# Performance work log

Hardware: AMD Instinct MI355X
Metric: run time of the kernel (lower is better)

The kernel has to match this reference:

```python
import jax, jax.numpy as jnp
import numpy as np

BATCH = 2
L = 2048
D_MODEL = 1024
D_STATE = 16
D_CONV = 4
EXPAND = 2
D_INNER = EXPAND * D_MODEL  # 2048
DT_RANK = (D_MODEL + 15) // 16  # 64


def setup_inputs() -> dict:
    key = jax.random.key(0)
    ks = jax.random.split(key, 12)
    f = jnp.float32
    hidden_states = jax.random.normal(ks[0], (BATCH, L, D_MODEL), f)
    input2 = jax.random.normal(ks[1], (BATCH, L, D_MODEL), f)
    in_proj1_w = jax.random.normal(ks[2], (D_INNER, D_MODEL), f) * (D_MODEL ** -0.5)
    in_proj2_w = jax.random.normal(ks[3], (D_INNER, D_MODEL), f) * (D_MODEL ** -0.5)
    conv_w = jax.random.normal(ks[4], (D_INNER, 1, D_CONV), f) * (D_CONV ** -0.5)
    conv_b = jax.random.normal(ks[5], (D_INNER,), f) * 0.02
    x_proj_w = jax.random.normal(ks[6], (DT_RANK + 2 * D_STATE, D_INNER), f) * (D_INNER ** -0.5)
    dt_std = DT_RANK ** -0.5
    dt_proj_w = jax.random.uniform(ks[7], (D_INNER, DT_RANK), f, -dt_std, dt_std)
    # dt bias init: inverse softplus of log-uniform dt in [1e-3, 1e-1]
    dt = jnp.exp(jax.random.uniform(ks[8], (D_INNER,), f) * (np.log(0.1) - np.log(0.001)) + np.log(0.001))
    dt = jnp.clip(dt, 1e-4, None)
    dt_proj_b = dt + jnp.log(-jnp.expm1(-dt))
    # A_log init: log(1..d_state) broadcast over channels
    A_log = jnp.log(jnp.broadcast_to(jnp.arange(1, D_STATE + 1, dtype=f), (D_INNER, D_STATE)))
    D = jnp.ones((D_INNER,), f)
    out_proj_w = jax.random.normal(ks[9], (D_MODEL, D_INNER), f) * (D_INNER ** -0.5)
    return dict(hidden_states=hidden_states, input2=input2, in_proj1_w=in_proj1_w,
                in_proj2_w=in_proj2_w, conv_w=conv_w, conv_b=conv_b, x_proj_w=x_proj_w,
                dt_proj_w=dt_proj_w, dt_proj_b=dt_proj_b, A_log=A_log, D=D,
                out_proj_w=out_proj_w)


def _forward(hidden_states, input2, in_proj1_w, in_proj2_w, conv_w, conv_b,
             x_proj_w, dt_proj_w, dt_proj_b, A_log, D, out_proj_w):
    # in_proj: (B,L,Dm) -> (B,d_inner,L)
    x = jnp.einsum('bld,ed->bel', hidden_states, in_proj1_w)
    z = jnp.einsum('bld,ed->bel', input2, in_proj2_w)
    # causal depthwise conv1d (left pad d_conv-1, equiv to torch pad+truncate) + SiLU
    xc = jax.lax.conv_general_dilated(x, conv_w, (1,), [(D_CONV - 1, 0)],
                                      dimension_numbers=('NCH', 'OIH', 'NCH'),
                                      feature_group_count=D_INNER)
    x = jax.nn.silu(xc + conv_b[None, :, None])
    # x_proj -> dt, B, C
    x_dbl = jnp.einsum('bel,re->brl', x, x_proj_w)  # (B, dt_rank+2n, L)
    dt = x_dbl[:, :DT_RANK]
    Bm = x_dbl[:, DT_RANK:DT_RANK + D_STATE]       # (B, n, L)
    Cm = x_dbl[:, DT_RANK + D_STATE:]               # (B, n, L)
    delta = jnp.einsum('brl,er->bel', dt, dt_proj_w)
    delta = jax.nn.softplus(delta + dt_proj_b[None, :, None])  # (B, d_inner, L)
    A = -jnp.exp(A_log)  # (d_inner, n)
    # selective scan over time (time-major for lax.scan)
    dlt = jnp.transpose(delta, (2, 0, 1))  # (L, B, d)
    u = jnp.transpose(x, (2, 0, 1))        # (L, B, d)
    Bt = jnp.transpose(Bm, (2, 0, 1))      # (L, B, n)
    Ct = jnp.transpose(Cm, (2, 0, 1))      # (L, B, n)

    def step(state, inp):
        d_t, u_t, B_t, C_t = inp
        dA = jnp.exp(d_t[..., None] * A)                        # (B, d, n)
        state = state * dA + (d_t * u_t)[..., None] * B_t[:, None, :]
        y_t = jnp.einsum('bdn,bn->bd', state, C_t)
        return state, y_t

    init = jnp.zeros((hidden_states.shape[0], D_INNER, D_STATE), x.dtype)
    _, ys = jax.lax.scan(step, init, (dlt, u, Bt, Ct))
    y = jnp.transpose(ys, (1, 2, 0)) + D[None, :, None] * x  # (B, d, L)
    y = y * jax.nn.silu(z)
    out = jnp.einsum('bel,de->bld', y, out_proj_w)  # out_proj, no bias
    return out


def reference(hidden_states, input2, in_proj1_w, in_proj2_w, conv_w, conv_b,
              x_proj_w, dt_proj_w, dt_proj_b, A_log, D, out_proj_w):
    return _forward(hidden_states, input2, in_proj1_w, in_proj2_w, conv_w, conv_b,
                    x_proj_w, dt_proj_w, dt_proj_b, A_log, D, out_proj_w)
```

## Files before the change

kernel.cpp:

```cpp
#include <hip/hip_runtime.h>
#include <cstddef>
#include <cmath>

#define BATCH 2
#define LSEQ 2048
#define DM 1024
#define DSTATE 16
#define DI 2048
#define DTR 64
#define XDR 96
#define NC 64
#define TC 32
#define PN (4096 * 96)

using f32x4 = __attribute__((ext_vector_type(4))) float;
using bf16x8 = __attribute__((ext_vector_type(8))) short;

__device__ __forceinline__ unsigned short f2bf(float f) {
  union { float f; unsigned int u; } c; c.f = f;
  unsigned int u = c.u;
  return (unsigned short)((u + 0x7FFFu + ((u >> 16) & 1u)) >> 16);
}
__device__ __forceinline__ float bf2f(unsigned short h) {
  union { unsigned int u; float f; } c; c.u = ((unsigned int)h) << 16;
  return c.f;
}
__device__ __forceinline__ unsigned int pack2(float a, float b) {
  return (unsigned int)f2bf(a) | ((unsigned int)f2bf(b) << 16);
}

__device__ __forceinline__ void gl_lds16(const void* g, void* l) {
  __builtin_amdgcn_global_load_lds(
      (const __attribute__((address_space(1))) void*)g,
      (__attribute__((address_space(3))) void*)l, 16, 0, 0);
}

__device__ __forceinline__ float softplus_fast(float x) {
  float ex = __expf(x);
  return (x > 20.f) ? x : __logf(1.f + ex);
}

__device__ __forceinline__ void pow_tree(float q1, float* dA) {
  float q2 = q1 * q1;
  float q3 = q2 * q1;
  float q4 = q2 * q2;
  float q8 = q4 * q4;
  float q5 = q4 * q1, q6 = q4 * q2, q7 = q4 * q3;
  dA[0] = q1;  dA[1] = q2;  dA[2] = q3;  dA[3] = q4;
  dA[4] = q5;  dA[5] = q6;  dA[6] = q7;  dA[7] = q8;
  dA[8] = q8 * q1;  dA[9] = q8 * q2;  dA[10] = q8 * q3;  dA[11] = q8 * q4;
  dA[12] = q8 * q5; dA[13] = q8 * q6; dA[14] = q8 * q7;  dA[15] = q8 * q8;
}

#define G_HS   524288
#define G_IN2  (G_HS + 524288)
#define G_W1   (G_IN2 + 262144)
#define G_W2   (G_W1 + 262144)
#define G_XPW  (G_W2 + 24576)
#define G_DTW  (G_XPW + 16384)
#define G_OW   (G_DTW + 262144)

__global__ __launch_bounds__(256) void cvt_all_kernel(
    const float* __restrict__ hs, const float* __restrict__ in2,
    const float* __restrict__ w1, const float* __restrict__ w2,
    const float* __restrict__ xpw, const float* __restrict__ dtw,
    const float* __restrict__ ow, unsigned short* __restrict__ hsb,
    unsigned short* __restrict__ in2b, unsigned short* __restrict__ wb1,
    unsigned short* __restrict__ wb2, unsigned short* __restrict__ xpwB,
    unsigned short* __restrict__ dtwB, unsigned short* __restrict__ owb) {
  int i = blockIdx.x * 256 + threadIdx.x;
  const float* s;
  unsigned short* d;
  int k;
  if (i < G_HS)       { s = hs;  d = hsb;  k = i; }
  else if (i < G_IN2) { s = in2; d = in2b; k = i - G_HS; }
  else if (i < G_W1)  { s = w1;  d = wb1;  k = i - G_IN2; }
  else if (i < G_W2)  { s = w2;  d = wb2;  k = i - G_W1; }
  else if (i < G_XPW) { s = xpw; d = xpwB; k = i - G_W2; }
  else if (i < G_DTW) { s = dtw; d = dtwB; k = i - G_XPW; }
  else                { s = ow;  d = owb;  k = i - G_DTW; }
  const float4* sp = reinterpret_cast<const float4*>(s) + (size_t)k * 2;
  float4 a = sp[0], b = sp[1];
  uint4 v = make_uint4(pack2(a.x, a.y), pack2(a.z, a.w), pack2(b.x, b.y),
                       pack2(b.z, b.w));
  *(reinterpret_cast<uint4*>(d) + k) = v;
}

__global__ __launch_bounds__(512) void gemm_in12(
    const unsigned short* __restrict__ A0, const unsigned short* __restrict__ B0,
    unsigned short* __restrict__ C0, const unsigned short* __restrict__ A1,
    const unsigned short* __restrict__ B1, unsigned short* __restrict__ C1) {
  __shared__ __align__(16) unsigned short Asm[2][256][64];
  __shared__ __align__(16) unsigned short Bsm[2][256][64];

  const unsigned short* A = blockIdx.z ? A1 : A0;
  const unsigned short* B = blockIdx.z ? B1 : B0;
  unsigned short* C = blockIdx.z ? C1 : C0;
  const int lda = DM, ldc = DI;

  const int tid = threadIdx.x;
  const int lane = tid & 63;
  const int w = tid >> 6;
  const int wr = w >> 2;
  const int wn = w & 3;

  const int gx = gridDim.x;
  const int nwg = gx * gridDim.y;
  const int id = blockIdx.y * gx + blockIdx.x;
  const int cpx = nwg >> 3;
  const int lt = (id & 7) * cpx + (id >> 3);
  const size_t m0 = (size_t)(lt / gx) * 256;
  const size_t n0 = (size_t)(lt % gx) * 256;

  const int rsub = lane >> 3;
  const int sslot = (lane & 7) ^ rsub;
  const unsigned short* Ab = A + (m0 + (size_t)rsub) * lda + sslot * 8;
  const unsigned short* Bb = B + (n0 + (size_t)rsub) * lda + sslot * 8;

  const int fr = lane & 15;
  const int q = lane >> 4;
  const int f7 = fr & 7;

  f32x4 acc[8][4] = {};
  bf16x8 bfr[4][2];

#define STA(BUF, T)                                                         \
  {                                                                         \
    const int r0_ = w * 32;                                                 \
    const unsigned short* s_ = Ab + (size_t)r0_ * lda + (T) * 64;           \
    gl_lds16(s_, &Asm[BUF][r0_][0]);                                        \
    gl_lds16(s_ + (size_t)8 * lda, &Asm[BUF][r0_ + 8][0]);                  \
    gl_lds16(s_ + (size_t)16 * lda, &Asm[BUF][r0_ + 16][0]);                \
    gl_lds16(s_ + (size_t)24 * lda, &Asm[BUF][r0_ + 24][0]);                \
  }
#define STB(BUF, T)                                                         \
  {                                                                         \
    const int r0_ = w * 32;                                                 \
    const unsigned short* s_ = Bb + (size_t)r0_ * lda + (T) * 64;           \
    gl_lds16(s_, &Bsm[BUF][r0_][0]);                                        \
    gl_lds16(s_ + (size_t)8 * lda, &Bsm[BUF][r0_ + 8][0]);                  \
    gl_lds16(s_ + (size_t)16 * lda, &Bsm[BUF][r0_ + 16][0]);                \
    gl_lds16(s_ + (size_t)24 * lda, &Bsm[BUF][r0_ + 24][0]);                \
  }

#define PH4(BUFI, HALF, LOADB, STG, VM)                                     \
  {                                                                         \
    if (LOADB) {                                                            \
      _Pragma("unroll") for (int j = 0; j < 4; ++j)                         \
          _Pragma("unroll") for (int kk = 0; kk < 2; ++kk)                  \
              bfr[j][kk] = *reinterpret_cast<const bf16x8*>(                \
                  &Bsm[BUFI][wn * 64 + j * 16 + fr]                         \
                      [((kk * 4 + q) ^ f7) << 3]);                          \
    }                                                                       \
    bf16x8 af_[4][2];                                                       \
    _Pragma("unroll") for (int mi = 0; mi < 4; ++mi)                        \
        _Pragma("unroll") for (int kk = 0; kk < 2; ++kk)                    \
            af_[mi][kk] = *reinterpret_cast<const bf16x8*>(                 \
                &Asm[BUFI][wr * 128 + ((HALF)*4 + mi) * 16 + fr]            \
                    [((kk * 4 + q) ^ f7) << 3]);                            \
    STG;                                                                    \
    VM;                                                                     \
    __builtin_amdgcn_s_barrier();                                           \
    asm volatile("s_waitcnt lgkmcnt(0)" ::: "memory");                      \
    __builtin_amdgcn_sched_barrier(0);                                      \
    __builtin_amdgcn_s_setprio(1);                                          \
    _Pragma("unroll") for (int kk = 0; kk < 2; ++kk)                        \
        _Pragma("unroll") for (int mi = 0; mi < 4; ++mi)                    \
            _Pragma("unroll") for (int j = 0; j < 4; ++j)                   \
                acc[(HALF)*4 + mi][j] =                                     \
                    __builtin_amdgcn_mfma_f32_16x16x32_bf16(                \
                        af_[mi][kk], bfr[j][kk], acc[(HALF)*4 + mi][j],     \
                        0, 0, 0);                                           \
    __builtin_amdgcn_s_setprio(0);                                          \
    __builtin_amdgcn_s_barrier();                                           \
  }

#define VMC4_ asm volatile("s_waitcnt vmcnt(4)" ::: "memory")
#define VMC0_ asm volatile("s_waitcnt vmcnt(0)" ::: "memory")
#define NOPS_ ((void)0)

  STB(0, 0)
  STA(0, 0)
  STB(1, 1)
  VMC4_;
  __builtin_amdgcn_s_barrier();

#pragma unroll 1
  for (int it = 0; it < 7; ++it) {
    const int t0 = 2 * it, t1 = 2 * it + 1;
    PH4(0, 0, true,  STA(1, t1),     NOPS_)
    PH4(0, 1, false, STB(0, t0 + 2), VMC4_)
    PH4(1, 0, true,  STA(0, t0 + 2), NOPS_)
    PH4(1, 1, false, STB(1, t1 + 2), VMC4_)
  }
  PH4(0, 0, true,  STA(1, 15), NOPS_)
  PH4(0, 1, false, NOPS_,      VMC0_)
  PH4(1, 0, true,  NOPS_, NOPS_)
  PH4(1, 1, false, NOPS_, NOPS_)

#undef STA
#undef STB
#undef PH4

  const int crb = q * 4;
#pragma unroll
  for (int mf = 0; mf < 8; ++mf) {
    size_t row = m0 + wr * 128 + mf * 16 + crb;
#pragma unroll
    for (int j = 0; j < 4; ++j) {
      size_t col = n0 + wn * 64 + j * 16 + fr;
#pragma unroll
      for (int r = 0; r < 4; ++r)
        C[(row + r) * ldc + col] = f2bf(acc[mf][j][r]);
    }
  }
}

__global__ __launch_bounds__(256) void gemm_out(
    const unsigned short* __restrict__ A, const unsigned short* __restrict__ B,
    float* __restrict__ C) {
  __shared__ __align__(16) unsigned short As[128][64];
  __shared__ __align__(16) unsigned short Bs[64][64];

  const int K = DI, lda = DI, ldb = DI, ldc = DM;

  const int tid = threadIdx.x;
  const int lane = tid & 63;
  const int w = tid >> 6;

  const int gx = gridDim.x;
  const int nwg = gx * gridDim.y;
  const int id = blockIdx.y * gx + blockIdx.x;
  const int cpx = nwg >> 3;
  const int lt = (id & 7) * cpx + (id >> 3);
  const size_t m0 = (size_t)(lt / gx) * 128;
  const size_t n0 = (size_t)(lt % gx) * 64;

  const int rsub = lane >> 3;
  const int sslot = (lane & 7) ^ rsub;
  const unsigned short* Ab = A + m0 * lda + (size_t)rsub * lda + sslot * 8;
  const unsigned short* Bb = B + n0 * ldb + (size_t)rsub * ldb + sslot * 8;

  f32x4 acc[4][2] = {};

  const int fr = lane & 15;
  const int q = lane >> 4;
  const int f7 = fr & 7;

  for (int k0 = 0; k0 < K; k0 += 64) {
#pragma unroll
    for (int i = 0; i < 4; ++i) {
      const int r0 = w * 32 + i * 8;
      gl_lds16(Ab + (size_t)r0 * lda + k0, &As[r0][0]);
    }
#pragma unroll
    for (int i = 0; i < 2; ++i) {
      const int r0 = w * 16 + i * 8;
      gl_lds16(Bb + (size_t)r0 * ldb + k0, &Bs[r0][0]);
    }
    __syncthreads();

    bf16x8 af[4][2], bf_[2][2];
#pragma unroll
    for (int kk = 0; kk < 2; ++kk) {
      const int sA = (((kk * 4 + q) ^ f7) << 3);
#pragma unroll
      for (int i = 0; i < 4; ++i)
        af[i][kk] = *reinterpret_cast<const bf16x8*>(
            &As[(w >> 1) * 64 + i * 16 + fr][sA]);
#pragma unroll
      for (int j = 0; j < 2; ++j)
        bf_[j][kk] = *reinterpret_cast<const bf16x8*>(
            &Bs[(w & 1) * 32 + j * 16 + fr][sA]);
    }
#pragma unroll
    for (int kk = 0; kk < 2; ++kk)
#pragma unroll
      for (int i = 0; i < 4; ++i)
#pragma unroll
        for (int j = 0; j < 2; ++j)
          acc[i][j] = __builtin_amdgcn_mfma_f32_16x16x32_bf16(
              af[i][kk], bf_[j][kk], acc[i][j], 0, 0, 0);
    __syncthreads();
  }

  const int crb = q * 4;
#pragma unroll
  for (int i = 0; i < 4; ++i) {
    size_t row = m0 + (w >> 1) * 64 + i * 16 + crb;
#pragma unroll
    for (int j = 0; j < 2; ++j) {
      size_t col = n0 + (w & 1) * 32 + j * 16 + fr;
#pragma unroll
      for (int r = 0; r < 4; ++r)
        C[(row + r) * ldc + col] = acc[i][j][r];
    }
  }
}

__global__ __launch_bounds__(256) void gemm_delta(
    const unsigned short* __restrict__ A, const unsigned short* __restrict__ B,
    const float* __restrict__ bias, unsigned short* __restrict__ C, int K,
    int lda, int ldb, int ldc) {
  __shared__ __align__(16) unsigned short As[128][64];
  __shared__ __align__(16) unsigned short Bs[128][64];

  const int tid = threadIdx.x;
  const int lane = tid & 63;
  const int w = tid >> 6;

  const int gx = gridDim.x;
  const int nwg = gx * gridDim.y;
  const int id = blockIdx.y * gx + blockIdx.x;
  const int cpx = nwg >> 3;
  const int lt = (id & 7) * cpx + (id >> 3);
  const size_t m0 = (size_t)(lt / gx) * 128;
  const size_t n0 = (size_t)(lt % gx) * 128;

  const int rsub = lane >> 3;
  const int sslot = (lane & 7) ^ rsub;
  const unsigned short* Ab = A + m0 * lda + (size_t)rsub * lda + sslot * 8;
  const unsigned short* Bb = B + n0 * ldb + (size_t)rsub * ldb + sslot * 8;

  f32x4 acc[4][4] = {};

  const int fr = lane & 15;
  const int q = lane >> 4;
  const int f7 = fr & 7;

  for (int k0 = 0; k0 < K; k0 += 64) {
#pragma unroll
    for (int i = 0; i < 4; ++i) {
      const int r0 = w * 32 + i * 8;
      gl_lds16(Ab + (size_t)r0 * lda + k0, &As[r0][0]);
      gl_lds16(Bb + (size_t)r0 * ldb + k0, &Bs[r0][0]);
    }
    __syncthreads();

    bf16x8 af[4][2], bf_[4][2];
#pragma unroll
    for (int i = 0; i < 4; ++i) {
#pragma unroll
      for (int kk = 0; kk < 2; ++kk) {
        const int sA = (((kk * 4 + q) ^ f7) << 3);
        af[i][kk] = *reinterpret_cast<const bf16x8*>(
            &As[(w >> 1) * 64 + i * 16 + fr][sA]);
        bf_[i][kk] = *reinterpret_cast<const bf16x8*>(
            &Bs[(w & 1) * 64 + i * 16 + fr][sA]);
      }
    }
#pragma unroll
    for (int kk = 0; kk < 2; ++kk)
#pragma unroll
      for (int i = 0; i < 4; ++i)
#pragma unroll
        for (int j = 0; j < 4; ++j)
          acc[i][j] = __builtin_amdgcn_mfma_f32_16x16x32_bf16(
              af[i][kk], bf_[j][kk], acc[i][j], 0, 0, 0);
    __syncthreads();
  }

  const int crb = q * 4;
#pragma unroll
  for (int i = 0; i < 4; ++i) {
    size_t row = m0 + (w >> 1) * 64 + i * 16 + crb;
#pragma unroll
    for (int j = 0; j < 4; ++j) {
      size_t col = n0 + (w & 1) * 64 + j * 16 + fr;
      float bv = bias[col];
#pragma unroll
      for (int r = 0; r < 4; ++r)
        C[(row + r) * ldc + col] = f2bf(softplus_fast(acc[i][j][r] + bv));
    }
  }
}

__global__ __launch_bounds__(256) void gemm_xdbl(
    const unsigned short* __restrict__ A,
    const unsigned short* __restrict__ B,
    float* __restrict__ P) {
  __shared__ __align__(16) unsigned short As[128][64];
  __shared__ __align__(16) unsigned short Bs[96][64];

  const int tid = threadIdx.x;
  const int lane = tid & 63;
  const int w = tid >> 6;
  const size_t m0 = (size_t)blockIdx.x * 128;
  const int k0base = blockIdx.y * 256;

  const int rsub = lane >> 3;
  const int sslot = (lane & 7) ^ rsub;
  const unsigned short* Ab = A + m0 * DI + (size_t)rsub * DI + sslot * 8;
  const unsigned short* Bb = B + (size_t)rsub * DI + sslot * 8;

  f32x4 acc[4][3] = {};

  const int fr = lane & 15;
  const int q = lane >> 4;
  const int f7 = fr & 7;

  for (int ks = 0; ks < 4; ++ks) {
    const int k0 = k0base + ks * 64;
#pragma unroll
    for (int i = 0; i < 4; ++i) {
      const int r0 = w * 32 + i * 8;
      gl_lds16(Ab + (size_t)r0 * DI + k0, &As[r0][0]);
    }
#pragma unroll
    for (int i = 0; i < 3; ++i) {
      const int r0 = w * 24 + i * 8;
      gl_lds16(Bb + (size_t)r0 * DI + k0, &Bs[r0][0]);
    }
    __syncthreads();

    bf16x8 af[4][2], bf_[3][2];
#pragma unroll
    for (int kk = 0; kk < 2; ++kk) {
      const int sA = (((kk * 4 + q) ^ f7) << 3);
#pragma unroll
      for (int i = 0; i < 4; ++i)
        af[i][kk] = *reinterpret_cast<const bf16x8*>(
            &As[(w >> 1) * 64 + i * 16 + fr][sA]);
#pragma unroll
      for (int j = 0; j < 3; ++j)
        bf_[j][kk] = *reinterpret_cast<const bf16x8*>(
            &Bs[(w & 1) * 48 + j * 16 + fr][sA]);
    }
#pragma unroll
    for (int kk = 0; kk < 2; ++kk)
#pragma unroll
      for (int i = 0; i < 4; ++i)
#pragma unroll
        for (int j = 0; j < 3; ++j)
          acc[i][j] = __builtin_amdgcn_mfma_f32_16x16x32_bf16(
              af[i][kk], bf_[j][kk], acc[i][j], 0, 0, 0);
    __syncthreads();
  }

  float* Pz = P + (size_t)blockIdx.y * PN;
  const int crb = q * 4;
#pragma unroll
  for (int i = 0; i < 4; ++i) {
    size_t row = m0 + (w >> 1) * 64 + i * 16 + crb;
#pragma unroll
    for (int j = 0; j < 3; ++j) {
      int col = (w & 1) * 48 + j * 16 + fr;
#pragma unroll
      for (int r = 0; r < 4; ++r) Pz[(row + r) * XDR + col] = acc[i][j][r];
    }
  }
}

__global__ __launch_bounds__(256) void reduce8x_kernel(
    const float* __restrict__ P, unsigned short* __restrict__ dtB,
    float* __restrict__ BC) {
  int i = blockIdx.x * 256 + threadIdx.x;
  int row = i / XDR, col = i - row * XDR;
  float s01 = P[i] + P[PN + i];
  float s23 = P[2 * PN + i] + P[3 * PN + i];
  float s45 = P[4 * PN + i] + P[5 * PN + i];
  float s67 = P[6 * PN + i] + P[7 * PN + i];
  float s = (s01 + s23) + (s45 + s67);
  if (col < 64)
    dtB[row * 64 + col] = f2bf(s);
  else
    BC[row * 32 + (col - 64)] = s;
}

__global__ __launch_bounds__(256) void conv_silu_kernel(
    const unsigned short* __restrict__ x, const float* __restrict__ w,
    const float* __restrict__ cb, unsigned short* __restrict__ out) {
  int idx = blockIdx.x * 256 + threadIdx.x;
  int e4 = idx % (DI / 4);
  int bl = idx / (DI / 4);
  int l = bl % LSEQ;
  int e = e4 * 4;

  const float4* cw = reinterpret_cast<const float4*>(w);
  float4 w0 = cw[e], w1 = cw[e + 1], w2 = cw[e + 2], w3 = cw[e + 3];
  float4 acc = *reinterpret_cast<const float4*>(&cb[e]);

#define TAPK(K, COMP)                                                       \
  {                                                                         \
    int ls = l - 3 + (K);                                                   \
    if (ls >= 0) {                                                          \
      uint2 xv = *reinterpret_cast<const uint2*>(                           \
          &x[((size_t)(bl) - 3 + (K)) * DI + e]);                           \
      acc.x = fmaf(bf2f((unsigned short)(xv.x & 0xffff)), w0.COMP, acc.x);  \
      acc.y = fmaf(bf2f((unsigned short)(xv.x >> 16)), w1.COMP, acc.y);     \
      acc.z = fmaf(bf2f((unsigned short)(xv.y & 0xffff)), w2.COMP, acc.z);  \
      acc.w = fmaf(bf2f((unsigned short)(xv.y >> 16)), w3.COMP, acc.w);     \
    }                                                                       \
  }
  TAPK(0, x)
  TAPK(1, y)
  TAPK(2, z)
  TAPK(3, w)
#undef TAPK

  acc.x = acc.x / (1.f + __expf(-acc.x));
  acc.y = acc.y / (1.f + __expf(-acc.y));
  acc.z = acc.z / (1.f + __expf(-acc.z));
  acc.w = acc.w / (1.f + __expf(-acc.w));
  *reinterpret_cast<uint2*>(&out[(size_t)bl * DI + e]) =
      make_uint2(pack2(acc.x, acc.y), pack2(acc.z, acc.w));
}

__global__ __launch_bounds__(256) void scan_passA(
    const unsigned short* __restrict__ dB, const unsigned short* __restrict__ u,
    const float* __restrict__ bc, const float* __restrict__ A_log,
    float* __restrict__ sEnd, float* __restrict__ sProd) {
  int g = blockIdx.x * 256 + threadIdx.x;
  int e = g & (DI - 1);
  int c = (g >> 11) & (NC - 1);
  int b = g >> 17;

  const float nA0 = -__expf(A_log[e * DSTATE]);
  bool aok = true;
#pragma unroll
  for (int n = 1; n < DSTATE; ++n) {
    float nAn = -__expf(A_log[e * DSTATE + n]);
    aok = aok && (fabsf(nAn - (float)(n + 1) * nA0) <= 1e-4f * fabsf(nAn));
  }

  size_t off = ((size_t)b * LSEQ + c * TC) * DI + e;
  size_t boff = ((size_t)b * LSEQ + c * TC) * 32;

  float s[DSTATE], P[DSTATE];
#pragma unroll
  for (int n = 0; n < DSTATE; ++n) { s[n] = 0.f; P[n] = 1.f; }
  float sumd = 0.f;

  float d = bf2f(dB[off]);
  float ut = bf2f(u[off]);

  for (int t = 0; t < TC; ++t) {
    float d_n = 0.f, ut_n = 0.f;
    if (t + 1 < TC) {
      d_n = bf2f(dB[off + DI]);
      ut_n = bf2f(u[off + DI]);
    }

    float db = d * ut;
    float dA[DSTATE];
    if (aok) {
      pow_tree(__expf(d * nA0), dA);
      sumd += d;
    } else {
#pragma unroll
      for (int n = 0; n < DSTATE; ++n) {
        dA[n] = __expf(-d * __expf(A_log[e * DSTATE + n]));
        P[n] *= dA[n];
      }
    }
    const float4* bcp = reinterpret_cast<const float4*>(&bc[boff]);
    float4 B0 = bcp[0], B1 = bcp[1], B2 = bcp[2], B3 = bcp[3];
    float Bv[DSTATE] = {B0.x, B0.y, B0.z, B0.w, B1.x, B1.y, B1.z, B1.w,
                        B2.x, B2.y, B2.z, B2.w, B3.x, B3.y, B3.z, B3.w};
#pragma unroll
    for (int n = 0; n < DSTATE; ++n)
      s[n] = fmaf(s[n], dA[n], db * Bv[n]);
    off += DI;
    boff += 32;
    d = d_n; ut = ut_n;
  }

  if (aok) pow_tree(__expf(sumd * nA0), P);

  size_t o = (((size_t)b * NC + c) * DI + e) * DSTATE;
  float4* se = reinterpret_cast<float4*>(&sEnd[o]);
  float4* sp = reinterpret_cast<float4*>(&sProd[o]);
  se[0] = make_float4(s[0], s[1], s[2], s[3]);
  se[1] = make_float4(s[4], s[5], s[6], s[7]);
  se[2] = make_float4(s[8], s[9], s[10], s[11]);
  se[3] = make_float4(s[12], s[13], s[14], s[15]);
  sp[0] = make_float4(P[0], P[1], P[2], P[3]);
  sp[1] = make_float4(P[4], P[5], P[6], P[7]);
  sp[2] = make_float4(P[8], P[9], P[10], P[11]);
  sp[3] = make_float4(P[12], P[13], P[14], P[15]);
}

__global__ __launch_bounds__(256) void scan_passB(
    float* __restrict__ sEnd, const float* __restrict__ sProd) {
  int g = blockIdx.x * 256 + threadIdx.x;
  int n = g & 15;
  int e = (g >> 4) & (DI - 1);
  int b = g >> 15;
  float s = 0.f;
  for (int c = 0; c < NC; ++c) {
    size_t o = (((size_t)b * NC + c) * DI + e) * DSTATE + n;
    float se = sEnd[o];
    float sp = sProd[o];
    sEnd[o] = s;
    s = fmaf(s, sp, se);
  }
}

__global__ __launch_bounds__(256) void scan_passC(
    const unsigned short* __restrict__ dB, const unsigned short* __restrict__ u,
    const unsigned short* __restrict__ z, const float* __restrict__ bc,
    const float* __restrict__ A_log, const float* __restrict__ Dv,
    const float* __restrict__ sInit, unsigned short* __restrict__ gOut) {
  int g = blockIdx.x * 256 + threadIdx.x;
  int e = g & (DI - 1);
  int c = (g >> 11) & (NC - 1);
  int b = g >> 17;

  const float nA0 = -__expf(A_log[e * DSTATE]);
  bool aok = true;
#pragma unroll
  for (int n = 1; n < DSTATE; ++n) {
    float nAn = -__expf(A_log[e * DSTATE + n]);
    aok = aok && (fabsf(nAn - (float)(n + 1) * nA0) <= 1e-4f * fabsf(nAn));
  }
  const float Dval = Dv[e];

  size_t off = ((size_t)b * LSEQ + c * TC) * DI + e;
  size_t boff = ((size_t)b * LSEQ + c * TC) * 32;

  float s[DSTATE];
  {
    size_t o = (((size_t)b * NC + c) * DI + e) * DSTATE;
    const float4* si = reinterpret_cast<const float4*>(&sInit[o]);
    float4 s0 = si[0], s1 = si[1], s2 = si[2], s3 = si[3];
    s[0] = s0.x; s[1] = s0.y; s[2] = s0.z; s[3] = s0.w;
    s[4] = s1.x; s[5] = s1.y; s[6] = s1.z; s[7] = s1.w;
    s[8] = s2.x; s[9] = s2.y; s[10] = s2.z; s[11] = s2.w;
    s[12] = s3.x; s[13] = s3.y; s[14] = s3.z; s[15] = s3.w;
  }

  float d = bf2f(dB[off]);
  float ut = bf2f(u[off]);
  float zt = bf2f(z[off]);

  for (int t = 0; t < TC; ++t) {
    float d_n = 0.f, ut_n = 0.f, zt_n = 0.f;
    if (t + 1 < TC) {
      d_n = bf2f(dB[off + DI]);
      ut_n = bf2f(u[off + DI]);
      zt_n = bf2f(z[off + DI]);
    }

    float db = d * ut;
    float dA[DSTATE];
    if (aok) {
      pow_tree(__expf(d * nA0), dA);
    } else {
#pragma unroll
      for (int n = 0; n < DSTATE; ++n)
        dA[n] = __expf(-d * __expf(A_log[e * DSTATE + n]));
    }
    const float4* bcp = reinterpret_cast<const float4*>(&bc[boff]);
    float4 B0 = bcp[0], B1 = bcp[1], B2 = bcp[2], B3 = bcp[3];
    float4 C0 = bcp[4], C1 = bcp[5], C2 = bcp[6], C3 = bcp[7];
    float Bv[DSTATE] = {B0.x, B0.y, B0.z, B0.w, B1.x, B1.y, B1.z, B1.w,
                        B2.x, B2.y, B2.z, B2.w, B3.x, B3.y, B3.z, B3.w};
    float Cv[DSTATE] = {C0.x, C0.y, C0.z, C0.w, C1.x, C1.y, C1.z, C1.w,
                        C2.x, C2.y, C2.z, C2.w, C3.x, C3.y, C3.z, C3.w};
    float y0 = 0.f, y1 = 0.f, y2 = 0.f, y3 = 0.f;
#pragma unroll
    for (int n = 0; n < 4; ++n) {
      s[n] = fmaf(s[n], dA[n], db * Bv[n]);
      y0 = fmaf(s[n], Cv[n], y0);
      s[n + 4] = fmaf(s[n + 4], dA[n + 4], db * Bv[n + 4]);
      y1 = fmaf(s[n + 4], Cv[n + 4], y1);
      s[n + 8] = fmaf(s[n + 8], dA[n + 8], db * Bv[n + 8]);
      y2 = fmaf(s[n + 8], Cv[n + 8], y2);
      s[n + 12] = fmaf(s[n + 12], dA[n + 12], db * Bv[n + 12]);
      y3 = fmaf(s[n + 12], Cv[n + 12], y3);
    }
    float y = (y0 + y1) + (y2 + y3);
    float gate = zt / (1.f + __expf(-zt));
    gOut[off] = f2bf((y + Dval * ut) * gate);

    off += DI;
    boff += 32;
    d = d_n; ut = ut_n; zt = zt_n;
  }
}

extern "C" void kernel_launch(void* const* d_in, const int* in_sizes, int n_in,
                              void* d_out, int out_size, void* d_ws,
                              size_t ws_size, hipStream_t stream) {
  const float* hs = (const float*)d_in[0];
  const float* in2 = (const float*)d_in[1];
  const float* w1 = (const float*)d_in[2];
  const float* w2 = (const float*)d_in[3];
  const float* cw = (const float*)d_in[4];
  const float* cb = (const float*)d_in[5];
  const float* xpw = (const float*)d_in[6];
  const float* dtw = (const float*)d_in[7];
  const float* dtb = (const float*)d_in[8];
  const float* alog = (const float*)d_in[9];
  const float* Dv = (const float*)d_in[10];
  const float* ow = (const float*)d_in[11];
  float* out = (float*)d_out;

  const size_t BLE = (size_t)BATCH * LSEQ * DI;
  const size_t WN = (size_t)DI * DM;
  const size_t SC = (size_t)BATCH * NC * DI * DSTATE;

  float* W = (float*)d_ws;
  float* bufX = W;
  float* M2 = W + BLE;
  float* M3 = M2 + BLE / 2;
  float* M4 = M3 + BLE / 2;
  float* sEnd = M4 + BLE / 2;
  float* sProd = sEnd + SC;
  float* BC = sProd + SC;
  float* DED = BC + 131072;

  unsigned short* xpreB = (unsigned short*)bufX;
  unsigned short* dB = (unsigned short*)bufX;
  unsigned short* hsb = (unsigned short*)M2;
  unsigned short* zb = (unsigned short*)M2;
  unsigned short* in2b = (unsigned short*)M3;
  unsigned short* ub = (unsigned short*)M3;
  unsigned short* wb1 = (unsigned short*)M4;
  unsigned short* wb2 = wb1 + WN;
  float* xdblP = M4;
  unsigned short* dtB = (unsigned short*)(M4 + 8 * PN);
  unsigned short* bufG = (unsigned short*)M4;
  unsigned short* owb = (unsigned short*)DED;
  unsigned short* xpwB = owb + WN;
  unsigned short* dtwB = xpwB + XDR * DI;

  const int M = BATCH * LSEQ;
  dim3 blk(256);

  cvt_all_kernel<<<G_OW / 256, blk, 0, stream>>>(hs, in2, w1, w2, xpw, dtw, ow,
                                                 hsb, in2b, wb1, wb2, xpwB,
                                                 dtwB, owb);
  gemm_in12<<<dim3(DI / 256, M / 256, 2), dim3(512), 0, stream>>>(
      hsb, wb1, xpreB, in2b, wb2, zb);
  conv_silu_kernel<<<(M * (DI / 4)) / 256, blk, 0, stream>>>(xpreB, cw, cb,
                                                             ub);
  gemm_xdbl<<<dim3(M / 128, 8), blk, 0, stream>>>(ub, xpwB, xdblP);
  reduce8x_kernel<<<(M * XDR) / 256, blk, 0, stream>>>(xdblP, dtB, BC);
  gemm_delta<<<dim3(DI / 128, M / 128), blk, 0, stream>>>(
      dtB, dtwB, dtb, dB, DTR, DTR, DTR, DI);
  scan_passA<<<(BATCH * DI * NC) / 256, blk, 0, stream>>>(dB, ub, BC, alog,
                                                          sEnd, sProd);
  scan_passB<<<(BATCH * DI * DSTATE) / 256, blk, 0, stream>>>(sEnd, sProd);
  scan_passC<<<(BATCH * DI * NC) / 256, blk, 0, stream>>>(
      dB, ub, zb, BC, alog, Dv, sEnd, bufG);
  gemm_out<<<dim3(DM / 64, M / 128), blk, 0, stream>>>(bufG, owb, out);
}
```

Before: 214.9 us.

## Double-buffer out-projection GEMM with 512-thread 256x64 tiles and prefetch pipeline

Rewrites gemm_out to use 512 threads on a 256x64 output tile with two LDS buffers, prefetching the next K-tiles while MFMAs run on the current one. Explicit waitcnt, barriers and setprio schedule the loads against the compute. The intent is to hide global load latency and halve the number of workgroups. The grid falls to 256 blocks, which may underfill the GPU, and the hand-tuned vmcnt values are fragile.

```diff
diff --git a/kernel.cpp b/kernel.cpp
--- a/kernel.cpp
+++ b/kernel.cpp
@@ -216,84 +216,114 @@
   }
 }
 
-__global__ __launch_bounds__(256) void gemm_out(
+__global__ __launch_bounds__(512) void gemm_out(
     const unsigned short* __restrict__ A, const unsigned short* __restrict__ B,
     float* __restrict__ C) {
-  __shared__ __align__(16) unsigned short As[128][64];
-  __shared__ __align__(16) unsigned short Bs[64][64];
-
-  const int K = DI, lda = DI, ldb = DI, ldc = DM;
+  __shared__ __align__(16) unsigned short Asm[2][256][64];
+  __shared__ __align__(16) unsigned short Bsm[2][64][64];
+
+  const int lda = DI, ldc = DM;
 
   const int tid = threadIdx.x;
   const int lane = tid & 63;
   const int w = tid >> 6;
+  const int wm = w >> 1;
+  const int wn = w & 1;
 
   const int gx = gridDim.x;
   const int nwg = gx * gridDim.y;
   const int id = blockIdx.y * gx + blockIdx.x;
   const int cpx = nwg >> 3;
   const int lt = (id & 7) * cpx + (id >> 3);
-  const size_t m0 = (size_t)(lt / gx) * 128;
+  const size_t m0 = (size_t)(lt / gx) * 256;
   const size_t n0 = (size_t)(lt % gx) * 64;
 
   const int rsub = lane >> 3;
   const int sslot = (lane & 7) ^ rsub;
-  const unsigned short* Ab = A + m0 * lda + (size_t)rsub * lda + sslot * 8;
-  const unsigned short* Bb = B + n0 * ldb + (size_t)rsub * ldb + sslot * 8;
-
-  f32x4 acc[4][2] = {};
+  const unsigned short* Ab = A + (m0 + (size_t)rsub) * lda + sslot * 8;
+  const unsigned short* Bb = B + (n0 + (size_t)rsub) * lda + sslot * 8;
 
   const int fr = lane & 15;
   const int q = lane >> 4;
   const int f7 = fr & 7;
 
-  for (int k0 = 0; k0 < K; k0 += 64) {
-#pragma unroll
-    for (int i = 0; i < 4; ++i) {
-      const int r0 = w * 32 + i * 8;
-      gl_lds16(Ab + (size_t)r0 * lda + k0, &As[r0][0]);
-    }
-#pragma unroll
-    for (int i = 0; i < 2; ++i) {
-      const int r0 = w * 16 + i * 8;
-      gl_lds16(Bb + (size_t)r0 * ldb + k0, &Bs[r0][0]);
-    }
-    __syncthreads();
-
-    bf16x8 af[4][2], bf_[2][2];
-#pragma unroll
-    for (int kk = 0; kk < 2; ++kk) {
-      const int sA = (((kk * 4 + q) ^ f7) << 3);
-#pragma unroll
-      for (int i = 0; i < 4; ++i)
-        af[i][kk] = *reinterpret_cast<const bf16x8*>(
-            &As[(w >> 1) * 64 + i * 16 + fr][sA]);
-#pragma unroll
-      for (int j = 0; j < 2; ++j)
-        bf_[j][kk] = *reinterpret_cast<const bf16x8*>(
-            &Bs[(w & 1) * 32 + j * 16 + fr][sA]);
-    }
-#pragma unroll
-    for (int kk = 0; kk < 2; ++kk)
-#pragma unroll
-      for (int i = 0; i < 4; ++i)
-#pragma unroll
-        for (int j = 0; j < 2; ++j)
-          acc[i][j] = __builtin_amdgcn_mfma_f32_16x16x32_bf16(
-              af[i][kk], bf_[j][kk], acc[i][j], 0, 0, 0);
-    __syncthreads();
-  }
+  f32x4 acc[4][2] = {};
+
+#define OSTA(BUF, T)                                                        \
+  {                                                                         \
+    const int r0_ = w * 32;                                                 \
+    const unsigned short* s_ = Ab + (size_t)r0_ * lda + (T) * 64;           \
+    gl_lds16(s_, &Asm[BUF][r0_][0]);                                        \
+    gl_lds16(s_ + (size_t)8 * lda, &Asm[BUF][r0_ + 8][0]);                  \
+    gl_lds16(s_ + (size_t)16 * lda, &Asm[BUF][r0_ + 16][0]);                \
+    gl_lds16(s_ + (size_t)24 * lda, &Asm[BUF][r0_ + 24][0]);                \
+  }
+#define OSTB(BUF, T)                                                        \
+  {                                                                         \
+    const int r0_ = w * 8;                                                  \
+    gl_lds16(Bb + (size_t)r0_ * lda + (T) * 64, &Bsm[BUF][r0_][0]);         \
+  }
+
+#define OPH(BUFI, STG, VM)                                                  \
+  {                                                                         \
+    bf16x8 af_[4][2], bf_[2][2];                                            \
+    _Pragma("unroll") for (int j = 0; j < 2; ++j)                           \
+        _Pragma("unroll") for (int kk = 0; kk < 2; ++kk)                    \
+            bf_[j][kk] = *reinterpret_cast<const bf16x8*>(                  \
+                &Bsm[BUFI][wn * 32 + j * 16 + fr]                           \
+                    [((kk * 4 + q) ^ f7) << 3]);                            \
+    _Pragma("unroll") for (int mi = 0; mi < 4; ++mi)                        \
+        _Pragma("unroll") for (int kk = 0; kk < 2; ++kk)                    \
+            af_[mi][kk] = *reinterpret_cast<const bf16x8*>(                 \
+                &Asm[BUFI][wm * 64 + mi * 16 + fr]                          \
+                    [((kk * 4 + q) ^ f7) << 3]);                            \
+    asm volatile("s_waitcnt lgkmcnt(0)" ::: "memory");                      \
+    __builtin_amdgcn_sched_barrier(0);                                      \
+    __builtin_amdgcn_s_barrier();                                           \
+    STG;                                                                    \
+    VM;                                                                     \
+    __builtin_amdgcn_s_barrier();                                           \
+    __builtin_amdgcn_s_setprio(1);                                          \
+    _Pragma("unroll") for (int kk = 0; kk < 2; ++kk)                        \
+        _Pragma("unroll") for (int mi = 0; mi < 4; ++mi)                    \
+            _Pragma("unroll") for (int j = 0; j < 2; ++j)                   \
+                acc[mi][j] = __builtin_amdgcn_mfma_f32_16x16x32_bf16(       \
+                    af_[mi][kk], bf_[j][kk], acc[mi][j], 0, 0, 0);          \
+    __builtin_amdgcn_s_setprio(0);                                          \
+  }
+
+#define OVMC5_ asm volatile("s_waitcnt vmcnt(5)" ::: "memory")
+#define OVMC0_ asm volatile("s_waitcnt vmcnt(0)" ::: "memory")
+#define ONOP_ ((void)0)
+
+  OSTA(0, 0) OSTB(0, 0)
+  OSTA(1, 1) OSTB(1, 1)
+  OVMC5_;
+  __builtin_amdgcn_s_barrier();
+
+#pragma unroll 1
+  for (int it = 0; it < 15; ++it) {
+    const int t0 = 2 * it, t1 = 2 * it + 1;
+    OPH(0, { OSTA(0, t0 + 2) OSTB(0, t0 + 2) }, OVMC5_)
+    OPH(1, { OSTA(1, t1 + 2) OSTB(1, t1 + 2) }, OVMC5_)
+  }
+  OPH(0, ONOP_, OVMC0_)
+  OPH(1, ONOP_, ONOP_)
+
+#undef OSTA
+#undef OSTB
+#undef OPH
 
   const int crb = q * 4;
 #pragma unroll
-  for (int i = 0; i < 4; ++i) {
-    size_t row = m0 + (w >> 1) * 64 + i * 16 + crb;
+  for (int mf = 0; mf < 4; ++mf) {
+    size_t row = m0 + wm * 64 + mf * 16 + crb;
 #pragma unroll
     for (int j = 0; j < 2; ++j) {
-      size_t col = n0 + (w & 1) * 32 + j * 16 + fr;
+      size_t col = n0 + wn * 32 + j * 16 + fr;
 #pragma unroll
       for (int r = 0; r < 4; ++r)
-        C[(row + r) * ldc + col] = acc[i][j][r];
+        C[(row + r) * ldc + col] = acc[mf][j][r];
     }
   }
 }
@@ -744,5 +774,5 @@
   scan_passB<<<(BATCH * DI * DSTATE) / 256, blk, 0, stream>>>(sEnd, sProd);
   scan_passC<<<(BATCH * DI * NC) / 256, blk, 0, stream>>>(
       dB, ub, zb, BC, alog, Dv, sEnd, bufG);
-  gemm_out<<<dim3(DM / 64, M / 128), blk, 0, stream>>>(bufG, owb, out);
-}
+  gemm_out<<<dim3(DM / 64, M / 256), dim3(512), 0, stream>>>(bufG, owb, out);
+}
```

After: 214.8 us, median of 2. No clear change (-0.1%).
